# Optimization experiments

Measured on AMD Instinct MI355X. Metric: run time of the kernel, lower is better.

The kernel has to match this reference:

```python
import jax, jax.numpy as jnp
import numpy as np

N, E = 50000, 800000
IN, H, C = 256, 8, 32  # heads=8, hidden_dim=32 -> out dim 256
NEG_SLOPE = 0.2
EPS = 1e-5


def setup_inputs() -> dict:
    key = jax.random.key(0)
    ks = jax.random.split(key, 6)
    x = jax.random.normal(ks[0], (N, IN), jnp.float32)
    edge_index = jax.random.randint(ks[1], (2, E), 0, N, dtype=jnp.int32)
    W = jax.random.normal(ks[2], (IN, H * C), jnp.float32) / np.sqrt(IN).astype(np.float32)
    att_src = jax.random.normal(ks[3], (H, C), jnp.float32) * 0.1
    att_dst = jax.random.normal(ks[4], (H, C), jnp.float32) * 0.1
    bias = jnp.zeros((H * C,), jnp.float32)
    gamma = jnp.ones((H * C,), jnp.float32)
    beta = jnp.zeros((H * C,), jnp.float32)
    return {"x": x, "edge_index": edge_index, "W": W, "att_src": att_src,
            "att_dst": att_dst, "bias": bias, "gamma": gamma, "beta": beta}


def reference(x, edge_index, W, att_src, att_dst, bias, gamma, beta):
    n = x.shape[0]
    # Linear projection -> per-head features [N, H, C]
    xl = (x @ W).reshape(n, H, C)
    # Per-node attention half-logits [N, H]
    a_src = jnp.einsum('nhc,hc->nh', xl, att_src)
    a_dst = jnp.einsum('nhc,hc->nh', xl, att_dst)
    # Add self loops (PyG GATConv default)
    loops = jnp.arange(n, dtype=edge_index.dtype)
    src = jnp.concatenate([edge_index[0], loops])  # [E+N]
    dst = jnp.concatenate([edge_index[1], loops])
    # Edge attention logits + segment softmax over destination neighborhoods
    logits = jax.nn.leaky_relu(a_src[src] + a_dst[dst], NEG_SLOPE)  # [E+N, H]
    seg_max = jax.ops.segment_max(logits, dst, num_segments=n)
    ex = jnp.exp(logits - seg_max[dst])
    denom = jax.ops.segment_sum(ex, dst, num_segments=n)
    alpha = ex / denom[dst]  # [E+N, H]
    # Weighted scatter-aggregation of source features
    msgs = xl[src] * alpha[:, :, None]  # [E+N, H, C]
    out = jax.ops.segment_sum(msgs, dst, num_segments=n).reshape(n, H * C) + bias
    # LayerNorm over feature dim
    mu = jnp.mean(out, axis=-1, keepdims=True)
    var = jnp.var(out, axis=-1, keepdims=True)
    return (out - mu) / jnp.sqrt(var + EPS) * gamma + beta
```

## Files before the change

### kernel.cpp

```cpp
#include <hip/hip_runtime.h>
#include <math.h>

#define NEG 0.2f
#define LNEPS 1e-5f

typedef __attribute__((ext_vector_type(8))) short bf16x8;
typedef __attribute__((ext_vector_type(8))) unsigned short u16x8;
typedef __attribute__((ext_vector_type(4))) float f32x4;

__device__ __forceinline__ float lrelu(float x){ return x > 0.f ? x : NEG*x; }

__device__ __forceinline__ short f2b(float f){
  unsigned u = __float_as_uint(f);
  unsigned r = u + 0x7fffu + ((u >> 16) & 1u);
  return (short)(r >> 16);
}
__device__ __forceinline__ float b2f(unsigned short u){
  return __uint_as_float(((unsigned)u) << 16);
}

__global__ __launch_bounds__(256) void wt_k(const float* __restrict__ W,
                                            unsigned short* __restrict__ WT){
  int idx = blockIdx.x*256 + threadIdx.x;
  int k = idx >> 8, c = idx & 255;
  WT[c*256 + k] = (unsigned short)f2b(W[idx]);
}

__device__ __forceinline__ void load_half(float4 nx[8], const float* p){
  #pragma unroll
  for (int s=0;s<4;s++){
    nx[2*s]   = *(const float4*)(p + s*32);
    nx[2*s+1] = *(const float4*)(p + s*32 + 4);
  }
}
__device__ __forceinline__ void cvt_half(bf16x8 af[4], const float4 nx[8]){
  #pragma unroll
  for (int s=0;s<4;s++){
    af[s][0]=f2b(nx[2*s].x);   af[s][1]=f2b(nx[2*s].y);
    af[s][2]=f2b(nx[2*s].z);   af[s][3]=f2b(nx[2*s].w);
    af[s][4]=f2b(nx[2*s+1].x); af[s][5]=f2b(nx[2*s+1].y);
    af[s][6]=f2b(nx[2*s+1].z); af[s][7]=f2b(nx[2*s+1].w);
  }
}

__global__ __launch_bounds__(256, 2) void mfma_gemm_k(const float* __restrict__ A,
    const unsigned short* __restrict__ WT, unsigned short* __restrict__ Cb,
    const float* __restrict__ att_src, const float* __restrict__ att_dst,
    float* __restrict__ a_src, float* __restrict__ a_dst, int M, int nTiles){
  int w   = threadIdx.x >> 6;
  int l   = threadIdx.x & 63;
  int l15 = l & 15;
  int kg  = l >> 4;
  int colbase = w*64;

  bf16x8 bfr[4][8];
  #pragma unroll
  for (int j=0;j<4;j++){
    const unsigned short* bp = WT + (size_t)(colbase + j*16 + l15)*256 + kg*8;
    #pragma unroll
    for (int ks=0;ks<8;ks++) bfr[j][ks] = *(const bf16x8*)(bp + ks*32);
  }
  float as_r[4], ad_r[4];
  #pragma unroll
  for (int j=0;j<4;j++){
    as_r[j] = att_src[colbase + j*16 + l15];
    ad_r[j] = att_dst[colbase + j*16 + l15];
  }

  int t = blockIdx.x;
  if (t >= nTiles) return;
  int row0 = t*16 + l15;
  const float* ap = A + (size_t)(row0 < M ? row0 : M-1)*256 + kg*8;
  float4 nx[8];
  load_half(nx, ap);

  while (t < nTiles){
    f32x4 acc[4];
    #pragma unroll
    for (int j=0;j<4;j++) acc[j] = (f32x4){0.f,0.f,0.f,0.f};
    bf16x8 af[4];

    cvt_half(af, nx);
    load_half(nx, ap + 128);
    #pragma unroll
    for (int s=0;s<4;s++)
      #pragma unroll
      for (int j=0;j<4;j++)
        acc[j] = __builtin_amdgcn_mfma_f32_16x16x32_bf16(af[s], bfr[j][s], acc[j], 0, 0, 0);

    int tn = t + gridDim.x;
    int rown = tn < nTiles ? tn*16 + l15 : row0;
    const float* apn = A + (size_t)(rown < M ? rown : M-1)*256 + kg*8;

    cvt_half(af, nx);
    load_half(nx, apn);
    #pragma unroll
    for (int s=0;s<4;s++)
      #pragma unroll
      for (int j=0;j<4;j++)
        acc[j] = __builtin_amdgcn_mfma_f32_16x16x32_bf16(af[s], bfr[j][4+s], acc[j], 0, 0, 0);

    int orow_base = t*16 + kg*4;
    #pragma unroll
    for (int j=0;j<4;j++)
      #pragma unroll
      for (int rr=0;rr<4;rr++){
        int orow = orow_base + rr;
        if (orow < M) Cb[(size_t)orow*256 + colbase + j*16 + l15] = (unsigned short)f2b(acc[j][rr]);
      }
    #pragma unroll
    for (int rr=0;rr<4;rr++){
      float p0s = acc[0][rr]*as_r[0] + acc[1][rr]*as_r[1];
      float p0d = acc[0][rr]*ad_r[0] + acc[1][rr]*ad_r[1];
      float p1s = acc[2][rr]*as_r[2] + acc[3][rr]*as_r[3];
      float p1d = acc[2][rr]*ad_r[2] + acc[3][rr]*ad_r[3];
      #pragma unroll
      for (int m=1;m<16;m<<=1){
        p0s += __shfl_xor(p0s,m); p0d += __shfl_xor(p0d,m);
        p1s += __shfl_xor(p1s,m); p1d += __shfl_xor(p1d,m);
      }
      int orow = orow_base + rr;
      if (l15==0 && orow < M){
        a_src[(size_t)orow*8 + 2*w]   = p0s;
        a_dst[(size_t)orow*8 + 2*w]   = p0d;
        a_src[(size_t)orow*8 + 2*w+1] = p1s;
        a_dst[(size_t)orow*8 + 2*w+1] = p1d;
      }
    }
    t = tn; row0 = rown; ap = apn;
  }
}

__global__ void dinit_k(int* __restrict__ deg, int n){
  int i = blockIdx.x*blockDim.x+threadIdx.x;
  if (i<n) deg[i]=1;
}

__global__ void deg_k(const int* __restrict__ dst, int* __restrict__ deg, int E){
  int e = blockIdx.x*blockDim.x+threadIdx.x;
  if (e<E) atomicAdd(&deg[dst[e]],1);
}

__global__ __launch_bounds__(1024) void scan1_k(const int* __restrict__ deg,
                                                int* __restrict__ off,
                                                int* __restrict__ bsum, int n){
  __shared__ int wsum[16];
  int tid=threadIdx.x, lane=tid&63, wid=tid>>6;
  int i = blockIdx.x*1024 + tid;
  int v = (i<n)?deg[i]:0;
  int x = v;
  #pragma unroll
  for (int s=1;s<64;s<<=1){ int t2=__shfl_up(x,s); if (lane>=s) x+=t2; }
  if (lane==63) wsum[wid]=x;
  __syncthreads();
  if (tid<16){
    int y=wsum[tid];
    #pragma unroll
    for (int s=1;s<16;s<<=1){ int t2=__shfl_up(y,s); if (tid>=s) y+=t2; }
    wsum[tid]=y;
  }
  __syncthreads();
  int prefix=(wid? wsum[wid-1]:0);
  if (i<n) off[i]=prefix + x - v;
  if (tid==0) bsum[blockIdx.x]=wsum[15];
}

__global__ void scan2_k(int* __restrict__ bsum, int nb, int* __restrict__ offn){
  int lane = threadIdx.x;
  int v = (lane<nb)?bsum[lane]:0;
  int x = v;
  #pragma unroll
  for (int s=1;s<64;s<<=1){ int t2=__shfl_up(x,s); if (lane>=s) x+=t2; }
  if (lane<nb) bsum[lane] = x - v;
  if (lane==63) *offn = x;
}

__global__ __launch_bounds__(1024) void scan3_k(int* __restrict__ off,
                                                const int* __restrict__ bsum, int n){
  int i = blockIdx.x*1024 + threadIdx.x;
  if (i<n) off[i] += bsum[blockIdx.x];
}

__global__ void self_k(const int* __restrict__ off, int* __restrict__ sorted,
                       int* __restrict__ cur, int n){
  int i = blockIdx.x*blockDim.x+threadIdx.x;
  if (i<n){ sorted[off[i]] = i; cur[i] = 1; }
}

__global__ void scatter_k(const int* __restrict__ src, const int* __restrict__ dst,
                          const int* __restrict__ off, int* __restrict__ cur,
                          int* __restrict__ sorted, int E){
  int e=blockIdx.x*blockDim.x+threadIdx.x;
  if (e<E){
    int d=dst[e];
    int pos=off[d]+atomicAdd(&cur[d],1);
    sorted[pos]=src[e];
  }
}

__global__ __launch_bounds__(256) void agg3_k(const unsigned short* __restrict__ xlb,
    const float* __restrict__ a_src, const float* __restrict__ a_dst,
    const int* __restrict__ off, const int* __restrict__ sorted,
    const float* __restrict__ bias, const float* __restrict__ gamma,
    const float* __restrict__ beta, float* __restrict__ out, int n){
  int node = blockIdx.x*4 + (threadIdx.x>>6);
  if (node >= n) return;
  int lane = threadIdx.x & 63;
  int half = lane >> 5;
  int sl   = lane & 31;
  int h    = sl >> 2;
  float adst = a_dst[(size_t)node*8 + h];
  int s0 = off[node], dd = off[node+1] - s0;

  float acc[8] = {0.f,0.f,0.f,0.f,0.f,0.f,0.f,0.f};
  float den = 0.f;

  int i = 0;
  for (; i+8 <= dd; i += 8){
    int s[4];
    #pragma unroll
    for (int j=0;j<4;j++) s[j] = sorted[s0 + i + 2*j + half];
    u16x8 u[4];
    #pragma unroll
    for (int j=0;j<4;j++) u[j] = *(const u16x8*)(xlb + (size_t)s[j]*256 + sl*8);
    float wv[4];
    #pragma unroll
    for (int j=0;j<4;j++) wv[j] = __expf(lrelu(a_src[(size_t)s[j]*8+h]+adst));
    #pragma unroll
    for (int j=0;j<4;j++){
      den += wv[j];
      #pragma unroll
      for (int k=0;k<8;k++) acc[k] += wv[j]*b2f((unsigned short)u[j][k]);
    }
  }
  for (; i < dd; i += 2){
    int idx = i + half;
    bool ok = idx < dd;
    int s1 = ok ? sorted[s0+idx] : node;
    u16x8 u1 = *(const u16x8*)(xlb + (size_t)s1*256 + sl*8);
    float w1 = ok ? __expf(lrelu(a_src[(size_t)s1*8+h]+adst)) : 0.f;
    den += w1;
    #pragma unroll
    for (int k=0;k<8;k++) acc[k] += w1*b2f((unsigned short)u1[k]);
  }

  den += __shfl_xor(den, 32);
  #pragma unroll
  for (int k=0;k<8;k++) acc[k] += __shfl_xor(acc[k], 32);

  float rd = 1.0f/den;
  float4 bia0 = *(const float4*)(bias + sl*8);
  float4 bia1 = *(const float4*)(bias + sl*8 + 4);
  float o[8];
  o[0]=acc[0]*rd+bia0.x; o[1]=acc[1]*rd+bia0.y; o[2]=acc[2]*rd+bia0.z; o[3]=acc[3]*rd+bia0.w;
  o[4]=acc[4]*rd+bia1.x; o[5]=acc[5]*rd+bia1.y; o[6]=acc[6]*rd+bia1.z; o[7]=acc[7]*rd+bia1.w;

  float sum=0.f, ssq=0.f;
  #pragma unroll
  for (int k=0;k<8;k++){ sum += o[k]; ssq += o[k]*o[k]; }
  #pragma unroll
  for (int s=1;s<32;s<<=1){ sum += __shfl_xor(sum,s); ssq += __shfl_xor(ssq,s); }
  float mean = sum*(1.0f/256.0f);
  float var  = ssq*(1.0f/256.0f) - mean*mean;
  float rstd = rsqrtf(var + LNEPS);

  int f = sl*8 + half*4;
  float4 g  = *(const float4*)(gamma + f);
  float4 be = *(const float4*)(beta + f);
  int kb = half*4;
  float4 ov;
  ov.x = (o[kb+0]-mean)*rstd*g.x+be.x;
  ov.y = (o[kb+1]-mean)*rstd*g.y+be.y;
  ov.z = (o[kb+2]-mean)*rstd*g.z+be.z;
  ov.w = (o[kb+3]-mean)*rstd*g.w+be.w;
  *(float4*)(out + (size_t)node*256 + f) = ov;
}

extern "C" void kernel_launch(void* const* d_in, const int* in_sizes, int n_in,
                              void* d_out, int out_size, void* d_ws, size_t ws_size,
                              hipStream_t stream){
  const float* x       = (const float*)d_in[0];
  const int*   ei      = (const int*)  d_in[1];
  const float* W       = (const float*)d_in[2];
  const float* att_src = (const float*)d_in[3];
  const float* att_dst = (const float*)d_in[4];
  const float* bias    = (const float*)d_in[5];
  const float* gamma   = (const float*)d_in[6];
  const float* beta    = (const float*)d_in[7];
  float* out = (float*)d_out;

  int N = in_sizes[0]/256;
  int E = in_sizes[1]/2;
  const int* srcp = ei;
  const int* dstp = ei + E;

  unsigned short* xlb = (unsigned short*)d_ws;
  float* a_src = (float*)(xlb + (size_t)N*256);
  float* a_dst = a_src + (size_t)N*8;
  int*   deg   = (int*)(a_dst + (size_t)N*8);
  int*   off   = deg + N;
  int*   cur   = off + N + 1;
  int*   sorted= cur + N;
  int*   bsum  = sorted + E + N;
  unsigned short* WT = (unsigned short*)(bsum + 1024);

  int nb = (N + 1023)/1024;
  int nTiles = (N + 15)/16;

  wt_k<<<256, 256, 0, stream>>>(W, WT);
  mfma_gemm_k<<<512, 256, 0, stream>>>(x, WT, xlb, att_src, att_dst, a_src, a_dst, N, nTiles);
  dinit_k<<<(N+255)/256, 256, 0, stream>>>(deg, N);
  deg_k<<<(E+255)/256, 256, 0, stream>>>(dstp, deg, E);
  scan1_k<<<nb, 1024, 0, stream>>>(deg, off, bsum, N);
  scan2_k<<<1, 64, 0, stream>>>(bsum, nb, off + N);
  scan3_k<<<nb, 1024, 0, stream>>>(off, bsum, N);
  self_k<<<(N+255)/256, 256, 0, stream>>>(off, sorted, cur, N);
  scatter_k<<<(E+255)/256, 256, 0, stream>>>(srcp, dstp, off, cur, sorted, E);
  agg3_k<<<(N+3)/4, 256, 0, stream>>>(xlb, a_src, a_dst, off, sorted, bias, gamma, beta, out, N);
}
```

Before: 209.7 us.

## Precompute edge attention weights in scatter pass and merge scan3 with self-loop kernel

Edge attention weights exp(leaky_relu(a_src+a_dst)) are now computed once per edge and per head while the CSR is built, then written into a sorted-order w8 array. The aggregation kernel reads those weights instead of gathering a_src and recomputing exp. The scan-offset fixup and self-loop insertion are merged into one kernel, which saves a launch. In exchange, scatter does extra random gathers of a_src/a_dst plus 32-byte writes per edge, and agg reads about 27 MB of weight data instead of doing a scattered 4-byte a_src gather. Softmax max subtraction is still omitted, as it was before.

```diff
diff --git a/kernel.cpp b/kernel.cpp
--- a/kernel.cpp
+++ b/kernel.cpp
@@ -175,32 +175,53 @@
   if (lane==63) *offn = x;
 }
 
-__global__ __launch_bounds__(1024) void scan3_k(int* __restrict__ off,
-                                                const int* __restrict__ bsum, int n){
+__global__ __launch_bounds__(1024) void scan3self_k(int* __restrict__ off,
+    const int* __restrict__ bsum, int* __restrict__ sorted, int* __restrict__ cur,
+    float* __restrict__ w8, const float* __restrict__ a_src,
+    const float* __restrict__ a_dst, int n){
   int i = blockIdx.x*1024 + threadIdx.x;
-  if (i<n) off[i] += bsum[blockIdx.x];
-}
-
-__global__ void self_k(const int* __restrict__ off, int* __restrict__ sorted,
-                       int* __restrict__ cur, int n){
-  int i = blockIdx.x*blockDim.x+threadIdx.x;
-  if (i<n){ sorted[off[i]] = i; cur[i] = 1; }
+  if (i>=n) return;
+  int o = off[i] + bsum[blockIdx.x];
+  off[i] = o;
+  sorted[o] = i;
+  cur[i] = 1;
+  const float4* as = (const float4*)(a_src + (size_t)i*8);
+  const float4* ad = (const float4*)(a_dst + (size_t)i*8);
+  float4 s0=as[0], s1=as[1], d0=ad[0], d1=ad[1];
+  float4 w0, w1;
+  w0.x=__expf(lrelu(s0.x+d0.x)); w0.y=__expf(lrelu(s0.y+d0.y));
+  w0.z=__expf(lrelu(s0.z+d0.z)); w0.w=__expf(lrelu(s0.w+d0.w));
+  w1.x=__expf(lrelu(s1.x+d1.x)); w1.y=__expf(lrelu(s1.y+d1.y));
+  w1.z=__expf(lrelu(s1.z+d1.z)); w1.w=__expf(lrelu(s1.w+d1.w));
+  *(float4*)(w8 + (size_t)o*8)     = w0;
+  *(float4*)(w8 + (size_t)o*8 + 4) = w1;
 }
 
 __global__ void scatter_k(const int* __restrict__ src, const int* __restrict__ dst,
                           const int* __restrict__ off, int* __restrict__ cur,
-                          int* __restrict__ sorted, int E){
+                          int* __restrict__ sorted, float* __restrict__ w8,
+                          const float* __restrict__ a_src,
+                          const float* __restrict__ a_dst, int E){
   int e=blockIdx.x*blockDim.x+threadIdx.x;
-  if (e<E){
-    int d=dst[e];
-    int pos=off[d]+atomicAdd(&cur[d],1);
-    sorted[pos]=src[e];
-  }
-}
-
-__global__ __launch_bounds__(256) void agg3_k(const unsigned short* __restrict__ xlb,
-    const float* __restrict__ a_src, const float* __restrict__ a_dst,
+  if (e>=E) return;
+  int s=src[e], d=dst[e];
+  int pos=off[d]+atomicAdd(&cur[d],1);
+  sorted[pos]=s;
+  const float4* as = (const float4*)(a_src + (size_t)s*8);
+  const float4* ad = (const float4*)(a_dst + (size_t)d*8);
+  float4 s0=as[0], s1=as[1], d0=ad[0], d1=ad[1];
+  float4 w0, w1;
+  w0.x=__expf(lrelu(s0.x+d0.x)); w0.y=__expf(lrelu(s0.y+d0.y));
+  w0.z=__expf(lrelu(s0.z+d0.z)); w0.w=__expf(lrelu(s0.w+d0.w));
+  w1.x=__expf(lrelu(s1.x+d1.x)); w1.y=__expf(lrelu(s1.y+d1.y));
+  w1.z=__expf(lrelu(s1.z+d1.z)); w1.w=__expf(lrelu(s1.w+d1.w));
+  *(float4*)(w8 + (size_t)pos*8)     = w0;
+  *(float4*)(w8 + (size_t)pos*8 + 4) = w1;
+}
+
+__global__ __launch_bounds__(256) void agg4_k(const unsigned short* __restrict__ xlb,
     const int* __restrict__ off, const int* __restrict__ sorted,
+    const float* __restrict__ w8,
     const float* __restrict__ bias, const float* __restrict__ gamma,
     const float* __restrict__ beta, float* __restrict__ out, int n){
   int node = blockIdx.x*4 + (threadIdx.x>>6);
@@ -209,7 +230,6 @@
   int half = lane >> 5;
   int sl   = lane & 31;
   int h    = sl >> 2;
-  float adst = a_dst[(size_t)node*8 + h];
   int s0 = off[node], dd = off[node+1] - s0;
 
   float acc[8] = {0.f,0.f,0.f,0.f,0.f,0.f,0.f,0.f};
@@ -217,15 +237,17 @@
 
   int i = 0;
   for (; i+8 <= dd; i += 8){
-    int s[4];
-    #pragma unroll
-    for (int j=0;j<4;j++) s[j] = sorted[s0 + i + 2*j + half];
+    int p[4], s[4];
+    #pragma unroll
+    for (int j=0;j<4;j++) p[j] = s0 + i + 2*j + half;
+    #pragma unroll
+    for (int j=0;j<4;j++) s[j] = sorted[p[j]];
+    float wv[4];
+    #pragma unroll
+    for (int j=0;j<4;j++) wv[j] = w8[(size_t)p[j]*8 + h];
     u16x8 u[4];
     #pragma unroll
     for (int j=0;j<4;j++) u[j] = *(const u16x8*)(xlb + (size_t)s[j]*256 + sl*8);
-    float wv[4];
-    #pragma unroll
-    for (int j=0;j<4;j++) wv[j] = __expf(lrelu(a_src[(size_t)s[j]*8+h]+adst));
     #pragma unroll
     for (int j=0;j<4;j++){
       den += wv[j];
@@ -236,9 +258,10 @@
   for (; i < dd; i += 2){
     int idx = i + half;
     bool ok = idx < dd;
-    int s1 = ok ? sorted[s0+idx] : node;
+    int p = s0 + idx;
+    int s1 = ok ? sorted[p] : node;
+    float w1 = ok ? w8[(size_t)p*8 + h] : 0.f;
     u16x8 u1 = *(const u16x8*)(xlb + (size_t)s1*256 + sl*8);
-    float w1 = ok ? __expf(lrelu(a_src[(size_t)s1*8+h]+adst)) : 0.f;
     den += w1;
     #pragma unroll
     for (int k=0;k<8;k++) acc[k] += w1*b2f((unsigned short)u1[k]);
@@ -303,6 +326,7 @@
   int*   sorted= cur + N;
   int*   bsum  = sorted + E + N;
   unsigned short* WT = (unsigned short*)(bsum + 1024);
+  float* w8    = (float*)(WT + 65536);
 
   int nb = (N + 1023)/1024;
   int nTiles = (N + 15)/16;
@@ -313,8 +337,7 @@
   deg_k<<<(E+255)/256, 256, 0, stream>>>(dstp, deg, E);
   scan1_k<<<nb, 1024, 0, stream>>>(deg, off, bsum, N);
   scan2_k<<<1, 64, 0, stream>>>(bsum, nb, off + N);
-  scan3_k<<<nb, 1024, 0, stream>>>(off, bsum, N);
-  self_k<<<(N+255)/256, 256, 0, stream>>>(off, sorted, cur, N);
-  scatter_k<<<(E+255)/256, 256, 0, stream>>>(srcp, dstp, off, cur, sorted, E);
-  agg3_k<<<(N+3)/4, 256, 0, stream>>>(xlb, a_src, a_dst, off, sorted, bias, gamma, beta, out, N);
-}
+  scan3self_k<<<nb, 1024, 0, stream>>>(off, bsum, sorted, cur, w8, a_src, a_dst, N);
+  scatter_k<<<(E+255)/256, 256, 0, stream>>>(srcp, dstp, off, cur, sorted, w8, a_src, a_dst, E);
+  agg4_k<<<(N+3)/4, 256, 0, stream>>>(xlb, off, sorted, w8, bias, gamma, beta, out, N);
+}
```

Measured after the change: 214.9 us. 1.02x slower.
